# Performance work log

Measured on AMD Instinct MI355X. Metric: run time of the kernel, lower is better.

Reference implementation:

```python
import jax, jax.numpy as jnp
import numpy as np

EPS = 1e-5

def _layer_norm(x, gamma, beta):
    mu = jnp.mean(x, axis=-1, keepdims=True)
    var = jnp.mean(jnp.square(x - mu), axis=-1, keepdims=True)
    return (x - mu) * jax.lax.rsqrt(var + EPS) * gamma + beta

def setup_inputs() -> dict:
    key = jax.random.key(0)
    ks = jax.random.split(key, 6)
    B, D, H = 8192, 1024, 1024
    x = jax.random.normal(ks[0], (B, D), dtype=jnp.float32)
    h0 = jax.random.normal(ks[1], (B, H), dtype=jnp.float32)
    c0 = jax.random.normal(ks[2], (B, H), dtype=jnp.float32)
    # learned params (orthogonal init approximated by scaled normal for reference purposes)
    weight_h = jax.random.normal(ks[3], (H, 4 * H), dtype=jnp.float32) / np.sqrt(H)
    weight_x = jax.random.normal(ks[4], (D, 4 * H), dtype=jnp.float32) / np.sqrt(D)
    bias = jnp.zeros((4 * H,), dtype=jnp.float32).at[:H].set(1.0)  # forget-gate bias init to 1
    ln1_g = jnp.ones((4 * H,), jnp.float32); ln1_b = jnp.zeros((4 * H,), jnp.float32)
    ln2_g = jnp.ones((4 * H,), jnp.float32); ln2_b = jnp.zeros((4 * H,), jnp.float32)
    ln3_g = jnp.ones((H,), jnp.float32); ln3_b = jnp.zeros((H,), jnp.float32)
    return {"x": x, "h0": h0, "c0": c0, "weight_h": weight_h, "weight_x": weight_x,
            "bias": bias, "ln1_g": ln1_g, "ln1_b": ln1_b, "ln2_g": ln2_g, "ln2_b": ln2_b,
            "ln3_g": ln3_g, "ln3_b": ln3_b}

def reference(x, h0, c0, weight_h, weight_x, bias, ln1_g, ln1_b, ln2_g, ln2_b, ln3_g, ln3_b):
    # gates: [B, 4H] = LN(h0 @ Wh) + LN(x @ Wx) + bias
    gates = _layer_norm(h0 @ weight_h, ln1_g, ln1_b) + _layer_norm(x @ weight_x, ln2_g, ln2_b) + bias
    H = h0.shape[-1]
    f_g, i_g, o_g, c_g = jnp.split(gates, 4, axis=1)  # forget, in, out, cell
    c1 = jax.nn.sigmoid(f_g) * c0 + jax.nn.sigmoid(i_g) * jnp.tanh(c_g)
    h1 = jax.nn.sigmoid(o_g) * jnp.tanh(_layer_norm(c1, ln3_g, ln3_b))
    return (h1, c1)
```

## Files before the change

kernel.cpp:

```cpp
#include <hip/hip_runtime.h>
#include <cstdint>

#define B_ROWS 8192
#define KDIM 1024
#define N4 4096

typedef __attribute__((ext_vector_type(8))) short short8;
typedef __attribute__((ext_vector_type(4))) float float4v;

__device__ __forceinline__ unsigned short f2bf(float f) {
  union { float f; unsigned int u; } v; v.f = f;
  unsigned int r = v.u + 0x7fffu + ((v.u >> 16) & 1u);
  return (unsigned short)(r >> 16);
}

__device__ __forceinline__ float bf2f(unsigned short s) {
  union { unsigned int u; float f; } v; v.u = ((unsigned int)s) << 16;
  return v.f;
}

__device__ __forceinline__ void async16(const unsigned short* g, unsigned short* l) {
  auto gp = (const __attribute__((address_space(1))) unsigned int*)(uintptr_t)g;
  auto lp = (__attribute__((address_space(3))) unsigned int*)(unsigned int)(uintptr_t)l;
  __builtin_amdgcn_global_load_lds(gp, lp, 16, 0, 0);
}

__device__ __forceinline__ float sigm(float v) { return 1.f / (1.f + expf(-v)); }


__global__ __launch_bounds__(256) void cast_bf16(const float* __restrict__ in0,
                                                 unsigned short* __restrict__ out0,
                                                 const float* __restrict__ in1,
                                                 unsigned short* __restrict__ out1) {
  const float* in = blockIdx.y ? in1 : in0;
  unsigned short* out = blockIdx.y ? out1 : out0;
  int i = (blockIdx.x * 256 + threadIdx.x) * 4;
  float4 v = *(const float4*)(in + i);
  ushort4 o;
  o.x = f2bf(v.x); o.y = f2bf(v.y); o.z = f2bf(v.z); o.w = f2bf(v.w);
  *(ushort4*)(out + i) = o;
}

__global__ __launch_bounds__(256) void transpose_cast(const float* __restrict__ W0,
                                                      unsigned short* __restrict__ Wt0,
                                                      const float* __restrict__ W1,
                                                      unsigned short* __restrict__ Wt1) {
  const float* W = blockIdx.z ? W1 : W0;
  unsigned short* Wt = blockIdx.z ? Wt1 : Wt0;
  __shared__ float tile[32][33];
  int n0 = blockIdx.x * 32;
  int k0 = blockIdx.y * 32;
  int tx = threadIdx.x & 31;
  int ty = threadIdx.x >> 5;
#pragma unroll
  for (int i = 0; i < 32; i += 8)
    tile[ty + i][tx] = W[(size_t)(k0 + ty + i) * N4 + n0 + tx];
  __syncthreads();
#pragma unroll
  for (int i = 0; i < 32; i += 8)
    Wt[(size_t)(n0 + ty + i) * KDIM + k0 + tx] = f2bf(tile[tx][ty + i]);
}


__global__ __launch_bounds__(512, 2) void gemm_bf16(
    const unsigned short* __restrict__ Ah, const unsigned short* __restrict__ Wth,
    unsigned short* __restrict__ Uh,
    const unsigned short* __restrict__ Ax, const unsigned short* __restrict__ Wtx,
    unsigned short* __restrict__ Ux, int row0) {
  const unsigned short* A; const unsigned short* W; unsigned short* U;
  if (blockIdx.z == 0) { A = Ah; W = Wth; U = Uh; } else { A = Ax; W = Wtx; U = Ux; }

  __shared__ unsigned short ldsA[2 * 256 * 64];
  __shared__ unsigned short ldsB[2 * 256 * 64];

  const int tid = threadIdx.x;
  const int wave = tid >> 6;
  const int lane = tid & 63;
  const int wm2 = wave >> 2;
  const int wn4 = wave & 3;

  const int gx = N4 / 256;
  const int nwg = gx * (int)gridDim.y;
  const int f = (int)blockIdx.y * gx + (int)blockIdx.x;
  const int qq = nwg >> 3, rr = nwg & 7;
  const int xcd = f & 7, idx = f >> 3;
  const int wg = (xcd < rr) ? (xcd * (qq + 1) + idx)
                            : (rr * (qq + 1) + (xcd - rr) * qq + idx);
  const int bx = wg & (gx - 1);
  const int by = wg / gx;

  const int m0 = row0 + by * 256;
  const int n0 = bx * 256;

  const int r8 = lane >> 3;
  const int c8 = lane & 7;
  const int g8 = ((c8 - r8) & 7) * 8;
  const int aE = (wave & 3) * 16 + (wave >> 2) * 128;
  const int aL = aE + 64;
  const int bE = (wave >> 1) * 64 + (wave & 1) * 16;
  const int bL = bE + 32;

  const unsigned short* gAe = A + (size_t)(m0 + aE + r8) * KDIM + g8;
  const unsigned short* gAl = A + (size_t)(m0 + aL + r8) * KDIM + g8;
  const unsigned short* gBe = W + (size_t)(n0 + bE + r8) * KDIM + g8;
  const unsigned short* gBl = W + (size_t)(n0 + bL + r8) * KDIM + g8;

  const int lq = lane & 15, lh = lane >> 4;
  const int offA0 = (wm2 * 128 + lq) * 64 + ((lh + lq) & 7) * 8;
  const int offA1 = (wm2 * 128 + lq) * 64 + ((4 + lh + lq) & 7) * 8;
  const int offB0 = (wn4 * 64 + lq) * 64 + ((lh + lq) & 7) * 8;
  const int offB1 = (wn4 * 64 + lq) * 64 + ((4 + lh + lq) & 7) * 8;

  float4v acc[8][4];
  float4v zero = {0.f, 0.f, 0.f, 0.f};
#pragma unroll
  for (int i = 0; i < 8; ++i)
#pragma unroll
    for (int j = 0; j < 4; ++j) acc[i][j] = zero;

  async16(gAe, ldsA + aE * 64);
  async16(gAe + 8 * KDIM, ldsA + (aE + 8) * 64);
  async16(gBe, ldsB + bE * 64);
  async16(gBe + 8 * KDIM, ldsB + (bE + 8) * 64);
  async16(gBl, ldsB + bL * 64);
  async16(gBl + 8 * KDIM, ldsB + (bL + 8) * 64);
  async16(gAl, ldsA + aL * 64);
  async16(gAl + 8 * KDIM, ldsA + (aL + 8) * 64);
  asm volatile("s_waitcnt vmcnt(4)\n\ts_barrier" ::: "memory");

  short8 aF[4][2], bF[4][2];

#pragma unroll 2
  for (int t = 0; t < KDIM / 64; ++t) {
    const unsigned short* sA = ldsA + (t & 1) * 16384;
    const unsigned short* sB = ldsB + (t & 1) * 16384;
    unsigned short* dA = (unsigned short*)ldsA + ((t + 1) & 1) * 16384;
    unsigned short* dB = (unsigned short*)ldsB + ((t + 1) & 1) * 16384;
    const int k2 = (t + 1) * 64;

#pragma unroll
    for (int mi = 0; mi < 4; ++mi) {
      aF[mi][0] = *(const short8*)(sA + offA0 + mi * 1024);
      aF[mi][1] = *(const short8*)(sA + offA1 + mi * 1024);
    }
#pragma unroll
    for (int ni = 0; ni < 2; ++ni) {
      bF[ni][0] = *(const short8*)(sB + offB0 + ni * 1024);
      bF[ni][1] = *(const short8*)(sB + offB1 + ni * 1024);
    }
    async16(gAe + k2, dA + aE * 64);
    async16(gAe + k2 + 8 * KDIM, dA + (aE + 8) * 64);
    __builtin_amdgcn_s_setprio(1);
#pragma unroll
    for (int kk = 0; kk < 2; ++kk)
#pragma unroll
      for (int mi = 0; mi < 4; ++mi)
#pragma unroll
        for (int ni = 0; ni < 2; ++ni)
          acc[mi][ni] = __builtin_amdgcn_mfma_f32_16x16x32_bf16(aF[mi][kk], bF[ni][kk], acc[mi][ni], 0, 0, 0);
    __builtin_amdgcn_s_setprio(0);
    asm volatile("s_waitcnt vmcnt(4)\n\ts_barrier" ::: "memory");

#pragma unroll
    for (int ni = 0; ni < 2; ++ni) {
      bF[2 + ni][0] = *(const short8*)(sB + offB0 + (2 + ni) * 1024);
      bF[2 + ni][1] = *(const short8*)(sB + offB1 + (2 + ni) * 1024);
    }
    async16(gBe + k2, dB + bE * 64);
    async16(gBe + k2 + 8 * KDIM, dB + (bE + 8) * 64);
    __builtin_amdgcn_s_setprio(1);
#pragma unroll
    for (int kk = 0; kk < 2; ++kk)
#pragma unroll
      for (int mi = 0; mi < 4; ++mi)
#pragma unroll
        for (int ni = 0; ni < 2; ++ni)
          acc[mi][2 + ni] = __builtin_amdgcn_mfma_f32_16x16x32_bf16(aF[mi][kk], bF[2 + ni][kk], acc[mi][2 + ni], 0, 0, 0);
    __builtin_amdgcn_s_setprio(0);
    asm volatile("s_waitcnt vmcnt(4)\n\ts_barrier" ::: "memory");

#pragma unroll
    for (int mi = 0; mi < 4; ++mi) {
      aF[mi][0] = *(const short8*)(sA + offA0 + (4 + mi) * 1024);
      aF[mi][1] = *(const short8*)(sA + offA1 + (4 + mi) * 1024);
    }
    async16(gBl + k2, dB + bL * 64);
    async16(gBl + k2 + 8 * KDIM, dB + (bL + 8) * 64);
    __builtin_amdgcn_s_setprio(1);
#pragma unroll
    for (int kk = 0; kk < 2; ++kk)
#pragma unroll
      for (int mi = 0; mi < 4; ++mi)
#pragma unroll
        for (int ni = 0; ni < 2; ++ni)
          acc[4 + mi][ni] = __builtin_amdgcn_mfma_f32_16x16x32_bf16(aF[mi][kk], bF[ni][kk], acc[4 + mi][ni], 0, 0, 0);
    __builtin_amdgcn_s_setprio(0);
    asm volatile("s_waitcnt vmcnt(4)\n\ts_barrier" ::: "memory");

    async16(gAl + k2, dA + aL * 64);
    async16(gAl + k2 + 8 * KDIM, dA + (aL + 8) * 64);
    __builtin_amdgcn_s_setprio(1);
#pragma unroll
    for (int kk = 0; kk < 2; ++kk)
#pragma unroll
      for (int mi = 0; mi < 4; ++mi)
#pragma unroll
        for (int ni = 0; ni < 2; ++ni)
          acc[4 + mi][2 + ni] = __builtin_amdgcn_mfma_f32_16x16x32_bf16(aF[mi][kk], bF[2 + ni][kk], acc[4 + mi][2 + ni], 0, 0, 0);
    __builtin_amdgcn_s_setprio(0);
    asm volatile("s_waitcnt vmcnt(4)\n\ts_barrier" ::: "memory");
  }
  asm volatile("s_waitcnt vmcnt(0)" ::: "memory");

  const int colc = lane & 15;
  const int rowq = (lane >> 4) * 4;
  unsigned short* Ub = U + (size_t)(by * 256 + wm2 * 128 + rowq) * N4 + n0 + wn4 * 64 + colc;
#pragma unroll
  for (int mi = 0; mi < 8; ++mi)
#pragma unroll
    for (int r = 0; r < 4; ++r) {
      unsigned short* Urow = Ub + (size_t)(mi * 16 + r) * N4;
#pragma unroll
      for (int ni = 0; ni < 4; ++ni) Urow[ni * 16] = f2bf(acc[mi][ni][r]);
    }
}


__global__ __launch_bounds__(256) void fused_ln_lstm(
    const unsigned short* __restrict__ Uh, const unsigned short* __restrict__ Ux,
    const float* __restrict__ c0, const float* __restrict__ bias,
    const float* __restrict__ g1, const float* __restrict__ b1,
    const float* __restrict__ g2, const float* __restrict__ b2,
    const float* __restrict__ g3, const float* __restrict__ b3,
    float* __restrict__ h1o, float* __restrict__ c1o, int row0) {
  const int t = threadIdx.x;
  const int lane = t & 63;
  const int wv = t >> 6;
  const size_t rloc = blockIdx.x;
  const size_t rabs = rloc + (size_t)row0;

  const ushort4* uh = (const ushort4*)(Uh + rloc * N4);
  const ushort4* ux = (const ushort4*)(Ux + rloc * N4);
  float4 cold = ((const float4*)(c0 + rabs * KDIM))[t];

  float4 vh[4], vx[4];
  float sh = 0.f, qh = 0.f, sx = 0.f, qx = 0.f;
#pragma unroll
  for (int k = 0; k < 4; ++k) {
    ushort4 au = uh[k * 256 + t];
    float4 a; a.x = bf2f(au.x); a.y = bf2f(au.y); a.z = bf2f(au.z); a.w = bf2f(au.w);
    vh[k] = a;
    sh += (a.x + a.y) + (a.z + a.w);
    qh += a.x * a.x + a.y * a.y + a.z * a.z + a.w * a.w;
    ushort4 bu = ux[k * 256 + t];
    float4 b; b.x = bf2f(bu.x); b.y = bf2f(bu.y); b.z = bf2f(bu.z); b.w = bf2f(bu.w);
    vx[k] = b;
    sx += (b.x + b.y) + (b.z + b.w);
    qx += b.x * b.x + b.y * b.y + b.z * b.z + b.w * b.w;
  }
  __shared__ float red[4][4];
#pragma unroll
  for (int o = 32; o > 0; o >>= 1) {
    sh += __shfl_down(sh, o); qh += __shfl_down(qh, o);
    sx += __shfl_down(sx, o); qx += __shfl_down(qx, o);
  }
  if (lane == 0) { red[wv][0] = sh; red[wv][1] = qh; red[wv][2] = sx; red[wv][3] = qx; }
  __syncthreads();
  sh = red[0][0] + red[1][0] + red[2][0] + red[3][0];
  qh = red[0][1] + red[1][1] + red[2][1] + red[3][1];
  sx = red[0][2] + red[1][2] + red[2][2] + red[3][2];
  qx = red[0][3] + red[1][3] + red[2][3] + red[3][3];
  const float inv4 = 1.f / 4096.f;
  const float muh = sh * inv4, mux = sx * inv4;
  const float rsh = rsqrtf(qh * inv4 - muh * muh + 1e-5f);
  const float rsx = rsqrtf(qx * inv4 - mux * mux + 1e-5f);

  float4 gate[4];
#pragma unroll
  for (int k = 0; k < 4; ++k) {
    int j = k * 256 + t;
    float4 G1 = ((const float4*)g1)[j], B1 = ((const float4*)b1)[j];
    float4 G2 = ((const float4*)g2)[j], B2 = ((const float4*)b2)[j];
    float4 BB = ((const float4*)bias)[j];
    float4 a = vh[k], b = vx[k], r;
    r.x = (a.x - muh) * rsh * G1.x + B1.x + (b.x - mux) * rsx * G2.x + B2.x + BB.x;
    r.y = (a.y - muh) * rsh * G1.y + B1.y + (b.y - mux) * rsx * G2.y + B2.y + BB.y;
    r.z = (a.z - muh) * rsh * G1.z + B1.z + (b.z - mux) * rsx * G2.z + B2.z + BB.z;
    r.w = (a.w - muh) * rsh * G1.w + B1.w + (b.w - mux) * rsx * G2.w + B2.w + BB.w;
    gate[k] = r;
  }
  float4 fg = gate[0], ig = gate[1], og = gate[2], cg = gate[3];
  float4 c1v;
  c1v.x = sigm(fg.x) * cold.x + sigm(ig.x) * tanhf(cg.x);
  c1v.y = sigm(fg.y) * cold.y + sigm(ig.y) * tanhf(cg.y);
  c1v.z = sigm(fg.z) * cold.z + sigm(ig.z) * tanhf(cg.z);
  c1v.w = sigm(fg.w) * cold.w + sigm(ig.w) * tanhf(cg.w);

  float sc = (c1v.x + c1v.y) + (c1v.z + c1v.w);
  float qc = c1v.x * c1v.x + c1v.y * c1v.y + c1v.z * c1v.z + c1v.w * c1v.w;
#pragma unroll
  for (int o = 32; o > 0; o >>= 1) { sc += __shfl_down(sc, o); qc += __shfl_down(qc, o); }
  __syncthreads();
  if (lane == 0) { red[wv][0] = sc; red[wv][1] = qc; }
  __syncthreads();
  sc = red[0][0] + red[1][0] + red[2][0] + red[3][0];
  qc = red[0][1] + red[1][1] + red[2][1] + red[3][1];
  const float invH = 1.f / 1024.f;
  const float muc = sc * invH;
  const float rsc = rsqrtf(qc * invH - muc * muc + 1e-5f);
  float4 G3 = ((const float4*)g3)[t], B3 = ((const float4*)b3)[t];
  float4 h1v;
  h1v.x = sigm(og.x) * tanhf((c1v.x - muc) * rsc * G3.x + B3.x);
  h1v.y = sigm(og.y) * tanhf((c1v.y - muc) * rsc * G3.y + B3.y);
  h1v.z = sigm(og.z) * tanhf((c1v.z - muc) * rsc * G3.z + B3.z);
  h1v.w = sigm(og.w) * tanhf((c1v.w - muc) * rsc * G3.w + B3.w);

  ((float4*)(h1o + rabs * KDIM))[t] = h1v;
  ((float4*)(c1o + rabs * KDIM))[t] = c1v;
}


extern "C" void kernel_launch(void* const* d_in, const int* in_sizes, int n_in,
                              void* d_out, int out_size, void* d_ws, size_t ws_size,
                              hipStream_t stream) {
  const float* x    = (const float*)d_in[0];
  const float* h0   = (const float*)d_in[1];
  const float* c0   = (const float*)d_in[2];
  const float* Wh   = (const float*)d_in[3];
  const float* Wx   = (const float*)d_in[4];
  const float* bias = (const float*)d_in[5];
  const float* g1   = (const float*)d_in[6];
  const float* b1   = (const float*)d_in[7];
  const float* g2   = (const float*)d_in[8];
  const float* b2   = (const float*)d_in[9];
  const float* g3   = (const float*)d_in[10];
  const float* b3   = (const float*)d_in[11];
  float* h1o = (float*)d_out;
  float* c1o = h1o + (size_t)B_ROWS * KDIM;

  unsigned short* Ah  = (unsigned short*)d_ws;
  unsigned short* Ax  = Ah + (size_t)B_ROWS * KDIM;
  unsigned short* Wth = Ax + (size_t)B_ROWS * KDIM;
  unsigned short* Wtx = Wth + (size_t)N4 * KDIM;
  unsigned short* U = Wtx + (size_t)N4 * KDIM;
  size_t used = ((size_t)B_ROWS * KDIM * 2 + (size_t)N4 * KDIM * 2) * sizeof(unsigned short);
  size_t rem = ws_size > used ? ws_size - used : 0;
  int chunk = (int)(rem / ((size_t)2 * N4 * sizeof(unsigned short)));
  chunk &= ~255;
  if (chunk > B_ROWS) chunk = B_ROWS;
  if (chunk < 256) chunk = 256;

  cast_bf16<<<dim3(B_ROWS * KDIM / 1024, 2), 256, 0, stream>>>(h0, Ah, x, Ax);
  transpose_cast<<<dim3(N4 / 32, KDIM / 32, 2), 256, 0, stream>>>(Wh, Wth, Wx, Wtx);

  for (int r0 = 0; r0 < B_ROWS; r0 += chunk) {
    int rows = chunk;
    if (r0 + rows > B_ROWS) rows = B_ROWS - r0;
    unsigned short* Uh = U;
    unsigned short* Ux = U + (size_t)rows * N4;
    gemm_bf16<<<dim3(N4 / 256, rows / 256, 2), 512, 0, stream>>>(Ah, Wth, Uh, Ax, Wtx, Ux, r0);
    fused_ln_lstm<<<rows, 256, 0, stream>>>(Uh, Ux, c0, bias, g1, b1, g2, b2, g3, b3, h1o, c1o, r0);
  }
}
```

Baseline: 372.2 us.

## Deepen GEMM prefetch pipeline to issue loads one extra K-step ahead

Restructures the double-buffered LDS pipeline so that A-even, B-even and B-late tile quarters for step t+2 are loaded into the current buffer as soon as each quarter is consumed. Only the A-late quarter goes to the other buffer for step t+1. The prologue preloads almost two stages and the wait counts rise to allow more loads in flight. One barrier per iteration is dropped. The aim is to hide more global memory latency, at the risk of subtle LDS hazards and out-of-range prefetch on the last iterations.

```diff
diff --git a/kernel.cpp b/kernel.cpp
--- a/kernel.cpp
+++ b/kernel.cpp
@@ -118,15 +118,20 @@
 #pragma unroll
     for (int j = 0; j < 4; ++j) acc[i][j] = zero;
 
-  async16(gAe, ldsA + aE * 64);
-  async16(gAe + 8 * KDIM, ldsA + (aE + 8) * 64);
-  async16(gBe, ldsB + bE * 64);
-  async16(gBe + 8 * KDIM, ldsB + (bE + 8) * 64);
-  async16(gBl, ldsB + bL * 64);
-  async16(gBl + 8 * KDIM, ldsB + (bL + 8) * 64);
-  async16(gAl, ldsA + aL * 64);
-  async16(gAl + 8 * KDIM, ldsA + (aL + 8) * 64);
-  asm volatile("s_waitcnt vmcnt(4)\n\ts_barrier" ::: "memory");
+#define STAGE2(gptr, lbase, kk)                                   \
+  do {                                                            \
+    async16((gptr) + (kk), (lbase));                              \
+    async16((gptr) + (kk) + 8 * KDIM, (lbase) + 8 * 64);          \
+  } while (0)
+
+  STAGE2(gAe, ldsA + aE * 64, 0);
+  STAGE2(gBe, ldsB + bE * 64, 0);
+  STAGE2(gBl, ldsB + bL * 64, 0);
+  STAGE2(gAl, ldsA + aL * 64, 0);
+  STAGE2(gAe, ldsA + 16384 + aE * 64, 64);
+  STAGE2(gBe, ldsB + 16384 + bE * 64, 64);
+  STAGE2(gBl, ldsB + 16384 + bL * 64, 64);
+  asm volatile("s_waitcnt vmcnt(10)\n\ts_barrier" ::: "memory");
 
   short8 aF[4][2], bF[4][2];
 
@@ -134,9 +139,11 @@
   for (int t = 0; t < KDIM / 64; ++t) {
     const unsigned short* sA = ldsA + (t & 1) * 16384;
     const unsigned short* sB = ldsB + (t & 1) * 16384;
-    unsigned short* dA = (unsigned short*)ldsA + ((t + 1) & 1) * 16384;
-    unsigned short* dB = (unsigned short*)ldsB + ((t + 1) & 1) * 16384;
-    const int k2 = (t + 1) * 64;
+    unsigned short* oA = (unsigned short*)ldsA + ((t + 1) & 1) * 16384;
+    unsigned short* cA = (unsigned short*)ldsA + (t & 1) * 16384;
+    unsigned short* cB = (unsigned short*)ldsB + (t & 1) * 16384;
+    const int kAL = (t + 1) * 64;
+    const int kNX = (t + 2) * 64;
 
 #pragma unroll
     for (int mi = 0; mi < 4; ++mi) {
@@ -148,8 +155,7 @@
       bF[ni][0] = *(const short8*)(sB + offB0 + ni * 1024);
       bF[ni][1] = *(const short8*)(sB + offB1 + ni * 1024);
     }
-    async16(gAe + k2, dA + aE * 64);
-    async16(gAe + k2 + 8 * KDIM, dA + (aE + 8) * 64);
+    STAGE2(gAl, oA + aL * 64, kAL);
     __builtin_amdgcn_s_setprio(1);
 #pragma unroll
     for (int kk = 0; kk < 2; ++kk)
@@ -159,15 +165,14 @@
         for (int ni = 0; ni < 2; ++ni)
           acc[mi][ni] = __builtin_amdgcn_mfma_f32_16x16x32_bf16(aF[mi][kk], bF[ni][kk], acc[mi][ni], 0, 0, 0);
     __builtin_amdgcn_s_setprio(0);
-    asm volatile("s_waitcnt vmcnt(4)\n\ts_barrier" ::: "memory");
+    asm volatile("s_waitcnt vmcnt(10)\n\ts_barrier" ::: "memory");
 
 #pragma unroll
     for (int ni = 0; ni < 2; ++ni) {
       bF[2 + ni][0] = *(const short8*)(sB + offB0 + (2 + ni) * 1024);
       bF[2 + ni][1] = *(const short8*)(sB + offB1 + (2 + ni) * 1024);
     }
-    async16(gBe + k2, dB + bE * 64);
-    async16(gBe + k2 + 8 * KDIM, dB + (bE + 8) * 64);
+    STAGE2(gAe, cA + aE * 64, kNX);
     __builtin_amdgcn_s_setprio(1);
 #pragma unroll
     for (int kk = 0; kk < 2; ++kk)
@@ -177,15 +182,14 @@
         for (int ni = 0; ni < 2; ++ni)
           acc[mi][2 + ni] = __builtin_amdgcn_mfma_f32_16x16x32_bf16(aF[mi][kk], bF[2 + ni][kk], acc[mi][2 + ni], 0, 0, 0);
     __builtin_amdgcn_s_setprio(0);
-    asm volatile("s_waitcnt vmcnt(4)\n\ts_barrier" ::: "memory");
+    asm volatile("s_waitcnt vmcnt(10)\n\ts_barrier" ::: "memory");
 
 #pragma unroll
     for (int mi = 0; mi < 4; ++mi) {
       aF[mi][0] = *(const short8*)(sA + offA0 + (4 + mi) * 1024);
       aF[mi][1] = *(const short8*)(sA + offA1 + (4 + mi) * 1024);
     }
-    async16(gBl + k2, dB + bL * 64);
-    async16(gBl + k2 + 8 * KDIM, dB + (bL + 8) * 64);
+    STAGE2(gBe, cB + bE * 64, kNX);
     __builtin_amdgcn_s_setprio(1);
 #pragma unroll
     for (int kk = 0; kk < 2; ++kk)
@@ -195,10 +199,7 @@
         for (int ni = 0; ni < 2; ++ni)
           acc[4 + mi][ni] = __builtin_amdgcn_mfma_f32_16x16x32_bf16(aF[mi][kk], bF[ni][kk], acc[4 + mi][ni], 0, 0, 0);
     __builtin_amdgcn_s_setprio(0);
-    asm volatile("s_waitcnt vmcnt(4)\n\ts_barrier" ::: "memory");
-
-    async16(gAl + k2, dA + aL * 64);
-    async16(gAl + k2 + 8 * KDIM, dA + (aL + 8) * 64);
+    STAGE2(gBl, cB + bL * 64, kNX);
     __builtin_amdgcn_s_setprio(1);
 #pragma unroll
     for (int kk = 0; kk < 2; ++kk)
@@ -208,7 +209,7 @@
         for (int ni = 0; ni < 2; ++ni)
           acc[4 + mi][2 + ni] = __builtin_amdgcn_mfma_f32_16x16x32_bf16(aF[mi][kk], bF[2 + ni][kk], acc[4 + mi][2 + ni], 0, 0, 0);
     __builtin_amdgcn_s_setprio(0);
-    asm volatile("s_waitcnt vmcnt(4)\n\ts_barrier" ::: "memory");
+    asm volatile("s_waitcnt vmcnt(10)\n\ts_barrier" ::: "memory");
   }
   asm volatile("s_waitcnt vmcnt(0)" ::: "memory");
 
```

New measurement: 359.5 us. 1.04x faster.
